# Kernel optimization log

Hardware: AMD Instinct MI355X
Metric: run time of the kernel (lower is better)

Reference implementation:

```python
import jax, jax.numpy as jnp
import numpy as np

N_TOTAL = 65536      # total nodes = NUM_GRAPHS * PER_GRAPH
NUM_GRAPHS = 1024
PER_GRAPH = 64       # num_nodes in module (per-graph)
E = 1048576          # edges, avg degree 16
IN_C = 128
HID_C = 128
OUT_C = 128
T = 8                # num_time_intervals
FC_OUT = T * PER_GRAPH * PER_GRAPH * 2  # 65536


def setup_inputs() -> dict:
    key = jax.random.key(0)
    ks = jax.random.split(key, 8)
    x = jax.random.normal(ks[0], (N_TOTAL, IN_C), dtype=jnp.float32)
    edge_index = jax.random.randint(ks[1], (2, E), 0, N_TOTAL, dtype=jnp.int64)
    batch = (jnp.arange(N_TOTAL, dtype=jnp.int64) // PER_GRAPH)  # graph id per node
    s = 0.05
    W1 = jax.random.normal(ks[2], (IN_C, HID_C), dtype=jnp.float32) * s
    b1 = jnp.zeros((HID_C,), dtype=jnp.float32)
    W2 = jax.random.normal(ks[3], (HID_C, OUT_C), dtype=jnp.float32) * s
    b2 = jnp.zeros((OUT_C,), dtype=jnp.float32)
    Wfc = jax.random.normal(ks[4], (OUT_C, FC_OUT), dtype=jnp.float32) * s
    bfc = jnp.zeros((FC_OUT,), dtype=jnp.float32)
    return {"x": x, "edge_index": edge_index, "batch": batch,
            "W1": W1, "b1": b1, "W2": W2, "b2": b2, "Wfc": Wfc, "bfc": bfc}


def reference(x, edge_index, batch, W1, b1, W2, b2, Wfc, bfc):
    n = x.shape[0]
    loop = jnp.arange(n)
    # GCNConv default: add self loops, symmetric normalization
    src = jnp.concatenate([edge_index[0], loop])
    dst = jnp.concatenate([edge_index[1], loop])
    deg = jax.ops.segment_sum(jnp.ones_like(dst, dtype=x.dtype), dst, num_segments=n)
    dinv = jnp.where(deg > 0, jax.lax.rsqrt(deg), 0.0)
    enorm = dinv[src] * dinv[dst]  # [E+n]

    def gcn(h, W, b):
        hw = h @ W                             # [n, C_out]
        msg = hw[src] * enorm[:, None]         # gather + per-edge scale
        return jax.ops.segment_sum(msg, dst, num_segments=n) + b

    h = jax.nn.relu(gcn(x, W1, b1))
    h = jax.nn.relu(gcn(h, W2, b2))

    # global_mean_pool over batch segments
    sums = jax.ops.segment_sum(h, batch, num_segments=NUM_GRAPHS)
    cnt = jax.ops.segment_sum(jnp.ones((n, 1), h.dtype), batch, num_segments=NUM_GRAPHS)
    pooled = sums / jnp.maximum(cnt, 1.0)

    out = pooled @ Wfc + bfc                   # [NUM_GRAPHS, FC_OUT]
    return out.reshape(-1, T, PER_GRAPH, PER_GRAPH * 2)
```

## Files before the change

### kernel.cpp

```cpp
#include <hip/hip_runtime.h>
#include <hip/hip_bf16.h>
#include <cstdint>

#define NODES  65536
#define CH     128
#define NGRAPH 1024
#define PGRAPH 64
#define FCO    65536

typedef __bf16 bf16x8 __attribute__((ext_vector_type(8)));
typedef __bf16 bf16x4 __attribute__((ext_vector_type(4)));
typedef float  f32x4  __attribute__((ext_vector_type(4)));

__device__ __forceinline__ float bflo(unsigned u){ return __uint_as_float(u << 16); }
__device__ __forceinline__ float bfhi(unsigned u){ return __uint_as_float(u & 0xffff0000u); }


__global__ void k_zero2(int* __restrict__ a, int* __restrict__ b){
  const int i = blockIdx.x*256 + threadIdx.x;
  ((int4*)a)[i] = make_int4(0,0,0,0);
  ((int4*)b)[i] = make_int4(0,0,0,0);
}

__global__ void k_degree(const int* __restrict__ dst, int* __restrict__ deg, int E){
  int e = blockIdx.x*256 + threadIdx.x;
  if (e < E) atomicAdd(&deg[dst[e]], 1);
}

__global__ void k_dinv(const int* __restrict__ deg, float* __restrict__ dinv){
  int i = blockIdx.x*256 + threadIdx.x;
  dinv[i] = 1.0f / sqrtf((float)(deg[i] + 1));
}

__global__ void k_scan1(const int* __restrict__ deg, int* __restrict__ excl,
                        int* __restrict__ bsums){
  __shared__ int tmp[256];
  const int t = threadIdx.x;
  const int gid = blockIdx.x*256 + t;
  const int v = deg[gid];
  tmp[t] = v;
  __syncthreads();
  #pragma unroll
  for (int off = 1; off < 256; off <<= 1){
    int x = (t >= off) ? tmp[t-off] : 0;
    __syncthreads();
    tmp[t] += x;
    __syncthreads();
  }
  excl[gid] = tmp[t] - v;
  if (t == 255) bsums[blockIdx.x] = tmp[255];
}

__global__ void k_scan2(int* __restrict__ bsums){
  __shared__ int tmp[256];
  const int t = threadIdx.x;
  const int v = bsums[t];
  tmp[t] = v;
  __syncthreads();
  #pragma unroll
  for (int off = 1; off < 256; off <<= 1){
    int x = (t >= off) ? tmp[t-off] : 0;
    __syncthreads();
    tmp[t] += x;
    __syncthreads();
  }
  bsums[t] = tmp[t] - v;
}

__global__ void k_scan3(int* __restrict__ cstart, const int* __restrict__ bsums, int E){
  const int gid = blockIdx.x*256 + threadIdx.x;
  cstart[gid] += bsums[blockIdx.x];
  if (gid == 0) cstart[NODES] = E;
}

__global__ void k_scatter(const int* __restrict__ src, const int* __restrict__ dst,
                          const int* __restrict__ cstart, int* __restrict__ cursor,
                          int* __restrict__ ssrc, int E){
  int e = blockIdx.x*256 + threadIdx.x;
  if (e >= E) return;
  const int d = dst[e];
  const int p = cstart[d] + atomicAdd(&cursor[d], 1);
  ssrc[p] = src[e];
}

template<int ABF>
__global__ __launch_bounds__(256)
void k_gemm128(const void* __restrict__ Av, const float* __restrict__ W,
               __bf16* __restrict__ Cout){
  __shared__ float As[128][36];
  __shared__ float Ws[32][160];
  const int t  = threadIdx.x;
  const int r0 = blockIdx.x * 128;
  const int q  = t & 3;
  const int rp = t >> 2;

  float acc0[32], acc1[32];
  #pragma unroll
  for (int j = 0; j < 32; ++j){ acc0[j] = 0.f; acc1[j] = 0.f; }

  for (int kc = 0; kc < 128; kc += 32){
    {
      const int row = t >> 1, u = t & 1;
      float* asp = &As[row][u*16];
      if (ABF){
        const __bf16* ap = (const __bf16*)Av + (size_t)(r0+row)*CH + kc + u*16;
        const bf16x8 v0 = *(const bf16x8*)ap;
        const bf16x8 v1 = *(const bf16x8*)(ap + 8);
        #pragma unroll
        for (int j = 0; j < 8; ++j){ asp[j] = (float)v0[j]; asp[8+j] = (float)v1[j]; }
      } else {
        const float* ap = (const float*)Av + (size_t)(r0+row)*CH + kc + u*16;
        #pragma unroll
        for (int i = 0; i < 4; ++i)
          *(float4*)(asp + 4*i) = *(const float4*)(ap + 4*i);
      }
    }
    {
      const int kk = t >> 3, u = t & 7;
      const float* wp = W + (size_t)(kc+kk)*CH + u*16;
      float* wsp = &Ws[kk][(u>>1)*40 + (u&1)*16];
      #pragma unroll
      for (int i = 0; i < 4; ++i)
        *(float4*)(wsp + 4*i) = *(const float4*)(wp + 4*i);
    }
    __syncthreads();

    #pragma unroll
    for (int kk4 = 0; kk4 < 8; ++kk4){
      const float4 a0 = *(const float4*)&As[rp][kk4*4];
      const float4 a1 = *(const float4*)&As[rp+64][kk4*4];
      const float a0f[4] = {a0.x, a0.y, a0.z, a0.w};
      const float a1f[4] = {a1.x, a1.y, a1.z, a1.w};
      #pragma unroll
      for (int kk = 0; kk < 4; ++kk){
        const float av0 = a0f[kk], av1 = a1f[kk];
        #pragma unroll
        for (int j4 = 0; j4 < 8; ++j4){
          const float4 w = *(const float4*)&Ws[kk4*4+kk][q*40 + j4*4];
          acc0[j4*4+0] = fmaf(av0, w.x, acc0[j4*4+0]);
          acc0[j4*4+1] = fmaf(av0, w.y, acc0[j4*4+1]);
          acc0[j4*4+2] = fmaf(av0, w.z, acc0[j4*4+2]);
          acc0[j4*4+3] = fmaf(av0, w.w, acc0[j4*4+3]);
          acc1[j4*4+0] = fmaf(av1, w.x, acc1[j4*4+0]);
          acc1[j4*4+1] = fmaf(av1, w.y, acc1[j4*4+1]);
          acc1[j4*4+2] = fmaf(av1, w.z, acc1[j4*4+2]);
          acc1[j4*4+3] = fmaf(av1, w.w, acc1[j4*4+3]);
        }
      }
    }
    __syncthreads();
  }

  __bf16* c0 = Cout + (size_t)(r0+rp)*CH    + q*32;
  __bf16* c1 = Cout + (size_t)(r0+rp+64)*CH + q*32;
  #pragma unroll
  for (int j4 = 0; j4 < 8; ++j4){
    bf16x4 v0, v1;
    #pragma unroll
    for (int e = 0; e < 4; ++e){ v0[e] = (__bf16)acc0[j4*4+e]; v1[e] = (__bf16)acc1[j4*4+e]; }
    *(bf16x4*)(c0 + j4*4) = v0;
    *(bf16x4*)(c1 + j4*4) = v1;
  }
}

__global__ __launch_bounds__(256)
void k_agg(const __bf16* __restrict__ hw, const float* __restrict__ dinv,
           const int* __restrict__ start, const int* __restrict__ srcs,
           const float* __restrict__ bias, __bf16* __restrict__ outp){
  const int l = threadIdx.x & 63, wave = threadIdx.x >> 6;
  const int n = l >> 4;
  const int q = l & 15;
  const int i = blockIdx.x*16 + wave*4 + n;
  const int c = q*8;
  const float di = dinv[i];

  const uint4 hs = *(const uint4*)&hw[(size_t)i*CH + c];
  float acc[8];
  acc[0] = di*bflo(hs.x); acc[1] = di*bfhi(hs.x);
  acc[2] = di*bflo(hs.y); acc[3] = di*bfhi(hs.y);
  acc[4] = di*bflo(hs.z); acc[5] = di*bfhi(hs.z);
  acc[6] = di*bflo(hs.w); acc[7] = di*bfhi(hs.w);

  int p = start[i];
  const int p1 = start[i+1];
  for (; p + 3 < p1; p += 4){
    const int s0 = srcs[p], s1 = srcs[p+1], s2 = srcs[p+2], s3 = srcs[p+3];
    const float w0 = dinv[s0], w1 = dinv[s1], w2 = dinv[s2], w3 = dinv[s3];
    const uint4 r0 = *(const uint4*)&hw[(size_t)s0*CH + c];
    const uint4 r1 = *(const uint4*)&hw[(size_t)s1*CH + c];
    const uint4 r2 = *(const uint4*)&hw[(size_t)s2*CH + c];
    const uint4 r3 = *(const uint4*)&hw[(size_t)s3*CH + c];
    acc[0]+=w0*bflo(r0.x); acc[1]+=w0*bfhi(r0.x); acc[2]+=w0*bflo(r0.y); acc[3]+=w0*bfhi(r0.y);
    acc[4]+=w0*bflo(r0.z); acc[5]+=w0*bfhi(r0.z); acc[6]+=w0*bflo(r0.w); acc[7]+=w0*bfhi(r0.w);
    acc[0]+=w1*bflo(r1.x); acc[1]+=w1*bfhi(r1.x); acc[2]+=w1*bflo(r1.y); acc[3]+=w1*bfhi(r1.y);
    acc[4]+=w1*bflo(r1.z); acc[5]+=w1*bfhi(r1.z); acc[6]+=w1*bflo(r1.w); acc[7]+=w1*bfhi(r1.w);
    acc[0]+=w2*bflo(r2.x); acc[1]+=w2*bfhi(r2.x); acc[2]+=w2*bflo(r2.y); acc[3]+=w2*bfhi(r2.y);
    acc[4]+=w2*bflo(r2.z); acc[5]+=w2*bfhi(r2.z); acc[6]+=w2*bflo(r2.w); acc[7]+=w2*bfhi(r2.w);
    acc[0]+=w3*bflo(r3.x); acc[1]+=w3*bfhi(r3.x); acc[2]+=w3*bflo(r3.y); acc[3]+=w3*bfhi(r3.y);
    acc[4]+=w3*bflo(r3.z); acc[5]+=w3*bfhi(r3.z); acc[6]+=w3*bflo(r3.w); acc[7]+=w3*bfhi(r3.w);
  }
  for (; p < p1; ++p){
    const int s = srcs[p];
    const float w = dinv[s];
    const uint4 r = *(const uint4*)&hw[(size_t)s*CH + c];
    acc[0]+=w*bflo(r.x); acc[1]+=w*bfhi(r.x); acc[2]+=w*bflo(r.y); acc[3]+=w*bfhi(r.y);
    acc[4]+=w*bflo(r.z); acc[5]+=w*bfhi(r.z); acc[6]+=w*bflo(r.w); acc[7]+=w*bfhi(r.w);
  }

  const float4 b0 = *(const float4*)&bias[c];
  const float4 b1 = *(const float4*)&bias[c+4];
  const float bb[8] = {b0.x,b0.y,b0.z,b0.w,b1.x,b1.y,b1.z,b1.w};
  bf16x8 o;
  #pragma unroll
  for (int k = 0; k < 8; ++k)
    o[k] = (__bf16)fmaxf(di*acc[k] + bb[k], 0.f);
  *(bf16x8*)&outp[(size_t)i*CH + c] = o;
}

__global__ void k_pool(const __bf16* __restrict__ h,
                       __bf16* __restrict__ phi, __bf16* __restrict__ plo){
  const int g = blockIdx.x, c = threadIdx.x;
  float acc = 0.f;
  const __bf16* hp = h + (size_t)g*PGRAPH*CH + c;
  #pragma unroll 4
  for (int i = 0; i < PGRAPH; ++i) acc += (float)hp[i*CH];
  const float v = acc * (1.0f/64.0f);
  const __bf16 hv = (__bf16)v;
  phi[g*CH + c] = hv;
  plo[g*CH + c] = (__bf16)(v - (float)hv);
}

__global__ __launch_bounds__(256)
void k_cvt_wfc(const float* __restrict__ Wfc, __bf16* __restrict__ wth,
               __bf16* __restrict__ wtl){
  __shared__ float ls[128][65];
  const int t  = threadIdx.x;
  const int c0 = blockIdx.x*64;

  #pragma unroll 8
  for (int it = 0; it < 32; ++it){
    const int row = it*4 + (t>>6);
    ls[row][t&63] = Wfc[(size_t)row*FCO + c0 + (t&63)];
  }
  __syncthreads();

  const int col = t>>2, q = t&3;
  const int tg  = (c0>>4) + (col>>4);
  const int lc  = col & 15;
  __bf16* dh = wth + (size_t)tg*2048 + q*512 + lc*8;
  __bf16* dl = wtl + (size_t)tg*2048 + q*512 + lc*8;
  #pragma unroll
  for (int i = 0; i < 4; ++i){
    bf16x8 h8, l8;
    #pragma unroll
    for (int j = 0; j < 8; ++j){
      const float v = ls[q*32 + i*8 + j][col];
      const __bf16 hv = (__bf16)v;
      h8[j] = hv;
      l8[j] = (__bf16)(v - (float)hv);
    }
    *(bf16x8*)(dh + i*128) = h8;
    *(bf16x8*)(dl + i*128) = l8;
  }
}

__global__ __launch_bounds__(256, 4)
void k_fc_mfma(const __bf16* __restrict__ phi, const __bf16* __restrict__ plo,
               const __bf16* __restrict__ wth, const __bf16* __restrict__ wtl,
               const float* __restrict__ bfc, float* __restrict__ out){
  const int t    = threadIdx.x;
  const int lane = t & 63, wave = t >> 6;
  const int lc   = lane & 15, kq = lane >> 4;
  const int g0   = blockIdx.y*32;
  const int c0w  = blockIdx.x*2048 + wave*512;

  bf16x8 ah[2][4], al[2][4];
  #pragma unroll
  for (int gt = 0; gt < 2; ++gt){
    const __bf16* pa = phi + (size_t)(g0 + gt*16 + lc)*CH + kq*8;
    const __bf16* pb = plo + (size_t)(g0 + gt*16 + lc)*CH + kq*8;
    #pragma unroll
    for (int kk = 0; kk < 4; ++kk){
      ah[gt][kk] = *(const bf16x8*)(pa + kk*32);
      al[gt][kk] = *(const bf16x8*)(pb + kk*32);
    }
  }

  const __bf16* bhp = wth + (size_t)(c0w >> 4)*2048 + lane*8;
  const __bf16* blp = wtl + (size_t)(c0w >> 4)*2048 + lane*8;
  float* o0 = out + (size_t)(g0 + lc)*FCO + c0w + kq*4;
  float* o1 = o0 + (size_t)16*FCO;
  const float* bp = bfc + c0w + kq*4;

  #pragma unroll 1
  for (int it = 0; it < 32; ++it){
    bf16x8 bh[4], bl[4];
    #pragma unroll
    for (int kk = 0; kk < 4; ++kk){
      bh[kk] = *(const bf16x8*)(bhp + kk*512);
      bl[kk] = *(const bf16x8*)(blp + kk*512);
    }
    f32x4 q0 = {0.f,0.f,0.f,0.f}, q1 = {0.f,0.f,0.f,0.f};
    #pragma unroll
    for (int kk = 0; kk < 4; ++kk){
      q0 = __builtin_amdgcn_mfma_f32_16x16x32_bf16(bh[kk], ah[0][kk], q0, 0,0,0);
      q1 = __builtin_amdgcn_mfma_f32_16x16x32_bf16(bh[kk], ah[1][kk], q1, 0,0,0);
      q0 = __builtin_amdgcn_mfma_f32_16x16x32_bf16(bl[kk], ah[0][kk], q0, 0,0,0);
      q1 = __builtin_amdgcn_mfma_f32_16x16x32_bf16(bl[kk], ah[1][kk], q1, 0,0,0);
      q0 = __builtin_amdgcn_mfma_f32_16x16x32_bf16(bh[kk], al[0][kk], q0, 0,0,0);
      q1 = __builtin_amdgcn_mfma_f32_16x16x32_bf16(bh[kk], al[1][kk], q1, 0,0,0);
    }
    const float4 b4 = *(const float4*)bp;
    float4 v;
    v.x = q0[0]+b4.x; v.y = q0[1]+b4.y; v.z = q0[2]+b4.z; v.w = q0[3]+b4.w;
    *(float4*)o0 = v;
    v.x = q1[0]+b4.x; v.y = q1[1]+b4.y; v.z = q1[2]+b4.z; v.w = q1[3]+b4.w;
    *(float4*)o1 = v;
    bhp += 2048; blp += 2048; o0 += 16; o1 += 16; bp += 16;
  }
}


extern "C" void kernel_launch(void* const* d_in, const int* in_sizes, int n_in,
                              void* d_out, int out_size, void* d_ws, size_t ws_size,
                              hipStream_t stream){
  const float* x   = (const float*)d_in[0];
  const int*   ei  = (const int*)d_in[1];
  const float* W1  = (const float*)d_in[3];
  const float* b1  = (const float*)d_in[4];
  const float* W2  = (const float*)d_in[5];
  const float* b2  = (const float*)d_in[6];
  const float* Wfc = (const float*)d_in[7];
  const float* bfc = (const float*)d_in[8];
  float* out = (float*)d_out;
  const int E = in_sizes[1] / 2;

  float* bufA   = (float*)d_ws;
  float* bufB   = bufA + (size_t)NODES*CH;
  float* dinv   = bufB + (size_t)NODES*CH;
  int*   deg    = (int*)(dinv + NODES);
  int*   cstart = deg + NODES;
  int*   cursor = cstart + NODES + 256;
  int*   bsums  = cursor + NODES;
  int*   ssrc   = bsums + 256;
  __bf16* phi   = (__bf16*)(ssrc + E);
  __bf16* plo   = phi + (size_t)NGRAPH*CH;

  __bf16* hwb = (__bf16*)bufA;
  __bf16* hbb = (__bf16*)bufB;
  __bf16* wth = (__bf16*)bufA;
  __bf16* wtl = wth + (size_t)FCO*CH;

  const int* esrc = ei;
  const int* edst = ei + E;

  k_zero2  <<<NODES/1024,  256, 0, stream>>>(deg, cursor);
  k_degree <<<(E+255)/256, 256, 0, stream>>>(edst, deg, E);
  k_dinv   <<<NODES/256,   256, 0, stream>>>(deg, dinv);
  k_scan1  <<<NODES/256,   256, 0, stream>>>(deg, cstart, bsums);
  k_scan2  <<<1,           256, 0, stream>>>(bsums);
  k_scan3  <<<NODES/256,   256, 0, stream>>>(cstart, bsums, E);
  k_scatter<<<(E+255)/256, 256, 0, stream>>>(esrc, edst, cstart, cursor, ssrc, E);

  k_gemm128<0><<<NODES/128, 256, 0, stream>>>(x,   W1, hwb);
  k_agg       <<<NODES/16, 256, 0, stream>>>(hwb, dinv, cstart, ssrc, b1, hbb);
  k_gemm128<1><<<NODES/128, 256, 0, stream>>>(hbb, W2, hwb);
  k_agg       <<<NODES/16, 256, 0, stream>>>(hwb, dinv, cstart, ssrc, b2, hbb);
  k_cvt_wfc <<<FCO/64, 256, 0, stream>>>(Wfc, wth, wtl);
  k_pool    <<<NGRAPH, CH, 0, stream>>>(hbb, phi, plo);
  k_fc_mfma <<<dim3(32, NGRAPH/32), 256, 0, stream>>>(phi, plo, wth, wtl, bfc, out);
}
```

Measured before the change: 415.8 us.

## Split feature matrix into four channel-quarter planes for cache-resident aggregation

Changes the intermediate node-feature layout from row-major [N,128] to four planes of [N,32] bf16, written by the GEMM and read by the pool kernel. Aggregation now runs as four launches, each gathering only one 4 MB plane, so the random neighbour gathers can stay in L2/LLC instead of streaming a 16 MB table. In exchange, each launch re-reads the CSR indices and dinv, issues 4-byte gathers instead of 16-byte ones, and adds launch overhead.

```diff
diff --git a/kernel.cpp b/kernel.cpp
--- a/kernel.cpp
+++ b/kernel.cpp
@@ -10,6 +10,7 @@
 
 typedef __bf16 bf16x8 __attribute__((ext_vector_type(8)));
 typedef __bf16 bf16x4 __attribute__((ext_vector_type(4)));
+typedef __bf16 bf16x2 __attribute__((ext_vector_type(2)));
 typedef float  f32x4  __attribute__((ext_vector_type(4)));
 
 __device__ __forceinline__ float bflo(unsigned u){ return __uint_as_float(u << 16); }
@@ -103,7 +104,8 @@
       const int row = t >> 1, u = t & 1;
       float* asp = &As[row][u*16];
       if (ABF){
-        const __bf16* ap = (const __bf16*)Av + (size_t)(r0+row)*CH + kc + u*16;
+        const __bf16* ap = (const __bf16*)Av
+            + ((size_t)(kc>>5)*NODES + r0 + row)*32 + u*16;
         const bf16x8 v0 = *(const bf16x8*)ap;
         const bf16x8 v1 = *(const bf16x8*)(ap + 8);
         #pragma unroll
@@ -151,79 +153,68 @@
     __syncthreads();
   }
 
-  __bf16* c0 = Cout + (size_t)(r0+rp)*CH    + q*32;
-  __bf16* c1 = Cout + (size_t)(r0+rp+64)*CH + q*32;
-  #pragma unroll
-  for (int j4 = 0; j4 < 8; ++j4){
-    bf16x4 v0, v1;
-    #pragma unroll
-    for (int e = 0; e < 4; ++e){ v0[e] = (__bf16)acc0[j4*4+e]; v1[e] = (__bf16)acc1[j4*4+e]; }
-    *(bf16x4*)(c0 + j4*4) = v0;
-    *(bf16x4*)(c1 + j4*4) = v1;
+  __bf16* c0 = Cout + ((size_t)q*NODES + r0 + rp)*32;
+  __bf16* c1 = Cout + ((size_t)q*NODES + r0 + rp + 64)*32;
+  #pragma unroll
+  for (int j8 = 0; j8 < 4; ++j8){
+    bf16x8 v0, v1;
+    #pragma unroll
+    for (int e = 0; e < 8; ++e){ v0[e] = (__bf16)acc0[j8*8+e]; v1[e] = (__bf16)acc1[j8*8+e]; }
+    *(bf16x8*)(c0 + j8*8) = v0;
+    *(bf16x8*)(c1 + j8*8) = v1;
   }
 }
 
 __global__ __launch_bounds__(256)
-void k_agg(const __bf16* __restrict__ hw, const float* __restrict__ dinv,
-           const int* __restrict__ start, const int* __restrict__ srcs,
-           const float* __restrict__ bias, __bf16* __restrict__ outp){
+void k_agg_q(const __bf16* __restrict__ hw0, const float* __restrict__ dinv,
+             const int* __restrict__ start, const int* __restrict__ srcs,
+             const float* __restrict__ bias, __bf16* __restrict__ out0, int q){
   const int l = threadIdx.x & 63, wave = threadIdx.x >> 6;
   const int n = l >> 4;
-  const int q = l & 15;
+  const int cq = (l & 15)*2;
   const int i = blockIdx.x*16 + wave*4 + n;
-  const int c = q*8;
   const float di = dinv[i];
 
-  const uint4 hs = *(const uint4*)&hw[(size_t)i*CH + c];
-  float acc[8];
-  acc[0] = di*bflo(hs.x); acc[1] = di*bfhi(hs.x);
-  acc[2] = di*bflo(hs.y); acc[3] = di*bfhi(hs.y);
-  acc[4] = di*bflo(hs.z); acc[5] = di*bfhi(hs.z);
-  acc[6] = di*bflo(hs.w); acc[7] = di*bfhi(hs.w);
+  const __bf16* hq = hw0 + (size_t)q*NODES*32;
+  const unsigned hs = *(const unsigned*)&hq[(size_t)i*32 + cq];
+  float ax = di*bflo(hs), ay = di*bfhi(hs);
 
   int p = start[i];
   const int p1 = start[i+1];
   for (; p + 3 < p1; p += 4){
     const int s0 = srcs[p], s1 = srcs[p+1], s2 = srcs[p+2], s3 = srcs[p+3];
     const float w0 = dinv[s0], w1 = dinv[s1], w2 = dinv[s2], w3 = dinv[s3];
-    const uint4 r0 = *(const uint4*)&hw[(size_t)s0*CH + c];
-    const uint4 r1 = *(const uint4*)&hw[(size_t)s1*CH + c];
-    const uint4 r2 = *(const uint4*)&hw[(size_t)s2*CH + c];
-    const uint4 r3 = *(const uint4*)&hw[(size_t)s3*CH + c];
-    acc[0]+=w0*bflo(r0.x); acc[1]+=w0*bfhi(r0.x); acc[2]+=w0*bflo(r0.y); acc[3]+=w0*bfhi(r0.y);
-    acc[4]+=w0*bflo(r0.z); acc[5]+=w0*bfhi(r0.z); acc[6]+=w0*bflo(r0.w); acc[7]+=w0*bfhi(r0.w);
-    acc[0]+=w1*bflo(r1.x); acc[1]+=w1*bfhi(r1.x); acc[2]+=w1*bflo(r1.y); acc[3]+=w1*bfhi(r1.y);
-    acc[4]+=w1*bflo(r1.z); acc[5]+=w1*bfhi(r1.z); acc[6]+=w1*bflo(r1.w); acc[7]+=w1*bfhi(r1.w);
-    acc[0]+=w2*bflo(r2.x); acc[1]+=w2*bfhi(r2.x); acc[2]+=w2*bflo(r2.y); acc[3]+=w2*bfhi(r2.y);
-    acc[4]+=w2*bflo(r2.z); acc[5]+=w2*bfhi(r2.z); acc[6]+=w2*bflo(r2.w); acc[7]+=w2*bfhi(r2.w);
-    acc[0]+=w3*bflo(r3.x); acc[1]+=w3*bfhi(r3.x); acc[2]+=w3*bflo(r3.y); acc[3]+=w3*bfhi(r3.y);
-    acc[4]+=w3*bflo(r3.z); acc[5]+=w3*bfhi(r3.z); acc[6]+=w3*bflo(r3.w); acc[7]+=w3*bfhi(r3.w);
+    const unsigned r0 = *(const unsigned*)&hq[(size_t)s0*32 + cq];
+    const unsigned r1 = *(const unsigned*)&hq[(size_t)s1*32 + cq];
+    const unsigned r2 = *(const unsigned*)&hq[(size_t)s2*32 + cq];
+    const unsigned r3 = *(const unsigned*)&hq[(size_t)s3*32 + cq];
+    ax += w0*bflo(r0); ay += w0*bfhi(r0);
+    ax += w1*bflo(r1); ay += w1*bfhi(r1);
+    ax += w2*bflo(r2); ay += w2*bfhi(r2);
+    ax += w3*bflo(r3); ay += w3*bfhi(r3);
   }
   for (; p < p1; ++p){
     const int s = srcs[p];
     const float w = dinv[s];
-    const uint4 r = *(const uint4*)&hw[(size_t)s*CH + c];
-    acc[0]+=w*bflo(r.x); acc[1]+=w*bfhi(r.x); acc[2]+=w*bflo(r.y); acc[3]+=w*bfhi(r.y);
-    acc[4]+=w*bflo(r.z); acc[5]+=w*bfhi(r.z); acc[6]+=w*bflo(r.w); acc[7]+=w*bfhi(r.w);
-  }
-
-  const float4 b0 = *(const float4*)&bias[c];
-  const float4 b1 = *(const float4*)&bias[c+4];
-  const float bb[8] = {b0.x,b0.y,b0.z,b0.w,b1.x,b1.y,b1.z,b1.w};
-  bf16x8 o;
-  #pragma unroll
-  for (int k = 0; k < 8; ++k)
-    o[k] = (__bf16)fmaxf(di*acc[k] + bb[k], 0.f);
-  *(bf16x8*)&outp[(size_t)i*CH + c] = o;
+    const unsigned r = *(const unsigned*)&hq[(size_t)s*32 + cq];
+    ax += w*bflo(r); ay += w*bfhi(r);
+  }
+
+  const float bx = bias[q*32 + cq], by = bias[q*32 + cq + 1];
+  bf16x2 o;
+  o[0] = (__bf16)fmaxf(di*ax + bx, 0.f);
+  o[1] = (__bf16)fmaxf(di*ay + by, 0.f);
+  *(bf16x2*)&out0[(size_t)q*NODES*32 + (size_t)i*32 + cq] = o;
 }
 
 __global__ void k_pool(const __bf16* __restrict__ h,
                        __bf16* __restrict__ phi, __bf16* __restrict__ plo){
   const int g = blockIdx.x, c = threadIdx.x;
+  const int qq = c >> 5, cw = c & 31;
   float acc = 0.f;
-  const __bf16* hp = h + (size_t)g*PGRAPH*CH + c;
+  const __bf16* hp = h + ((size_t)qq*NODES + (size_t)g*PGRAPH)*32 + cw;
   #pragma unroll 4
-  for (int i = 0; i < PGRAPH; ++i) acc += (float)hp[i*CH];
+  for (int i = 0; i < PGRAPH; ++i) acc += (float)hp[i*32];
   const float v = acc * (1.0f/64.0f);
   const __bf16 hv = (__bf16)v;
   phi[g*CH + c] = hv;
@@ -363,9 +354,12 @@
   k_scatter<<<(E+255)/256, 256, 0, stream>>>(esrc, edst, cstart, cursor, ssrc, E);
 
   k_gemm128<0><<<NODES/128, 256, 0, stream>>>(x,   W1, hwb);
-  k_agg       <<<NODES/16, 256, 0, stream>>>(hwb, dinv, cstart, ssrc, b1, hbb);
+  for (int q = 0; q < 4; ++q)
+    k_agg_q<<<NODES/16, 256, 0, stream>>>(hwb, dinv, cstart, ssrc, b1, hbb, q);
   k_gemm128<1><<<NODES/128, 256, 0, stream>>>(hbb, W2, hwb);
-  k_agg       <<<NODES/16, 256, 0, stream>>>(hwb, dinv, cstart, ssrc, b2, hbb);
+  for (int q = 0; q < 4; ++q)
+    k_agg_q<<<NODES/16, 256, 0, stream>>>(hwb, dinv, cstart, ssrc, b2, hbb, q);
+
   k_cvt_wfc <<<FCO/64, 256, 0, stream>>>(Wfc, wth, wtl);
   k_pool    <<<NGRAPH, CH, 0, stream>>>(hbb, phi, plo);
   k_fc_mfma <<<dim3(32, NGRAPH/32), 256, 0, stream>>>(phi, plo, wth, wtl, bfc, out);
```

After: 490.7 us. +18.0%, slower.
